# Optimization experiments

Hardware: AMD Instinct MI355X
Metric: run time of the kernel (lower is better)

The kernel has to match this reference:

```python
import jax, jax.numpy as jnp
import numpy as np

V = 32            # number_variables
K = 16            # degree + 1 spline coefficients per pair
DEG = 3           # cubic B-spline order for basis evaluation
LO, HI = -5.0, 5.0
SPAN_FACTOR = 0.1
N_SAMPLES = 131072
P_PAIRS = V * (V - 1) // 2  # 496


def bspline_basis(x):
    """Cubic B-spline basis with K clamped-uniform basis functions on the
    span_factor-expanded range [LO - s, HI + s].  x: [N] -> [N, K]."""
    s = SPAN_FACTOR * (HI - LO)
    lo, hi = LO - s, HI + s
    n_break = K - DEG + 1
    inner = jnp.linspace(lo, hi, n_break)
    t = jnp.concatenate([jnp.full((DEG,), lo), inner, jnp.full((DEG,), hi)])  # [K+DEG+1]
    x = jnp.clip(x, lo, hi - 1e-6 * (hi - lo))
    xb = x[:, None]
    # order-0 indicator functions: [N, K+DEG]
    B = ((xb >= t[None, :-1]) & (xb < t[None, 1:])).astype(x.dtype)
    for r in range(1, DEG + 1):
        tl, tr = t[:-(r + 1)], t[r:-1]
        den1 = tr - tl
        left = jnp.where(den1 > 0, (xb - tl) / jnp.where(den1 > 0, den1, 1.0), 0.0)
        tl2, tr2 = t[1:-r], t[r + 1:]
        den2 = tr2 - tl2
        right = jnp.where(den2 > 0, (tr2 - xb) / jnp.where(den2 > 0, den2, 1.0), 0.0)
        B = left * B[:, :-1] + right * B[:, 1:]
    return B  # [N, K]


def setup_inputs() -> dict:
    key = jax.random.key(0)
    k1, k2 = jax.random.split(key)
    inp = jax.random.normal(k1, (N_SAMPLES, V), dtype=jnp.float32)
    # learned spline coefficients, one column per (var, covar) pair,
    # initialized near the module's 0.1 constant init
    params = 0.1 + 0.05 * jax.random.normal(k2, (K, P_PAIRS), dtype=jnp.float32)
    return {"input": inp, "params": params}


def reference(input, params):
    # output[:, v] = input[:, v] + sum_{c < v} lambda_{v,c}(input[:, c]) * input[:, c]
    # In forward (non-inverse) mode every lambda depends only on `input`, so all
    # V*(V-1)/2 pairs are computed in one batched contraction instead of a loop.
    Basis = jax.vmap(bspline_basis)(input.T)  # [V, N, K], basis per covariate column
    idx_v, idx_c = np.tril_indices(V, -1)      # pair order matches params_index = v*(v-1)/2 + c
    P_mat = jnp.zeros((V, K, V), dtype=input.dtype).at[idx_c, :, idx_v].set(params.T)
    contrib = jnp.einsum('cnk,ckv->cnv', Basis, P_mat)   # lambda_{v,c}(x_{n,c})
    out = input + jnp.einsum('cnv,nc->nv', contrib, input)
    return out
```

## Files before the change

### kernel.cpp

```cpp
#include <hip/hip_runtime.h>
#include <hip/hip_bf16.h>


#define PPAIR 496

typedef _Float16 f16x8 __attribute__((ext_vector_type(8)));
typedef float f32x4 __attribute__((ext_vector_type(4)));
typedef unsigned int u32;
typedef unsigned int u32x4 __attribute__((ext_vector_type(4)));

__global__ __launch_bounds__(256) void prep_w2t(const float* __restrict__ params,
                                                unsigned short* __restrict__ w2t) {
    int idx = blockIdx.x * 256 + threadIdx.x;
    int v = idx >> 9;
    int c = (idx >> 4) & 31, k = idx & 15;
    float w = 0.0f;
    if (c < v) w = params[k * PPAIR + (v * (v - 1)) / 2 + c];
    _Float16 h = (_Float16)w;
    w2t[idx] = __builtin_bit_cast(unsigned short, h);
}

__global__ __launch_bounds__(256, 2) void decor_main(const float* __restrict__ xin,
                                                     const unsigned short* __restrict__ w2t,
                                                     float* __restrict__ out) {
    const int tid = threadIdx.x;
    const int wv = tid >> 6;
    const int l = tid & 63;
    const int s = l & 15;
    const int q = l >> 4;
    const int qp = q & 1;
    const int sigma = ((q & 1) << 1) | (q >> 1);

    f16x8 b1[8][2];
    f16x8 b0[4][2];
#pragma unroll
    for (int u = 0; u < 8; ++u) {
#pragma unroll
        for (int e = 0; e < 2; ++e) {
            int t = 2 * u + (qp ? (1 - e) : e);
            b1[u][e] = *(const f16x8*)(w2t + (16 + s) * 512 + t * 32 + q * 8);
            if (u < 4) b0[u][e] = *(const f16x8*)(w2t + s * 512 + t * 32 + q * 8);
        }
    }

    const float xmax = 5.999988f;
    const float sc = 13.0f / 12.0f;

    for (int tile = 0; tile < 4; ++tile) {
        const int S0 = blockIdx.x * 256 + wv * 64 + tile * 16;
        const float* xrow = xin + (S0 + s) * 32 + sigma;
        float xv[8];
#pragma unroll
        for (int u = 0; u < 8; ++u) xv[u] = xrow[4 * u];

        f32x4 acc0 = {0.f, 0.f, 0.f, 0.f};
        f32x4 acc1 = {0.f, 0.f, 0.f, 0.f};

#pragma unroll
        for (int u = 0; u < 8; ++u) {
            float x = xv[u];
            float xc = fminf(fmaxf(x, -6.0f), xmax);
            float uu = fmaf(xc, sc, 6.5f);
            int mi = (int)uu;
            mi = mi < 12 ? mi : 12;
            float mf = (float)mi;
            float r = uu - mf;
            float N0, N1, N2, N3;
            if (__all(mi >= 3 && mi <= 9)) {
                float omr = 1.0f - r;
                float r2 = r * r, r3 = r2 * r;
                float o2 = omr * omr;
                N0 = o2 * omr * (1.0f / 6.0f);
                N3 = r3 * (1.0f / 6.0f);
                N1 = fmaf(0.5f, r3, (2.0f / 3.0f) - r2);
                N2 = 1.0f - N0 - N1 - N3;
            } else {
                float t13 = 13.0f - mf;
                float af = fminf(mf, 1.0f);
                float bf = fminf(mf, 2.0f);
                float cf = fminf(t13, 2.0f);
                float df = fminf(t13, 3.0f);
                float r1 = 1.0f - r;
                float l2 = r + af, rr2 = cf - r;
                float l3 = r + bf, rr3 = df - r;
                float iv = (af == 0.0f) ? 1.0f : 0.5f;
                float T = r1 * iv;
                float M0 = r1 * T;
                float sv = l2 * T;
                float iv2 = (cf == 1.0f) ? 1.0f : 0.5f;
                float T2 = r * iv2;
                float M1 = fmaf(rr2, T2, sv);
                float M2 = r * T2;
                float iv3 = 0.5f;
                iv3 = (bf == 0.0f) ? 1.0f : iv3;
                iv3 = (bf == 2.0f) ? (1.0f / 3.0f) : iv3;
                T = M0 * iv3;
                N0 = r1 * T;
                sv = l3 * T;
                float g14 = af + cf;
                float iv4 = (g14 == 2.0f) ? 0.5f : (1.0f / 3.0f);
                T = M1 * iv4;
                N1 = fmaf(rr2, T, sv);
                sv = l2 * T;
                float iv5 = 0.5f;
                iv5 = (df == 1.0f) ? 1.0f : iv5;
                iv5 = (df == 3.0f) ? (1.0f / 3.0f) : iv5;
                T = M2 * iv5;
                N2 = fmaf(rr3, T, sv);
                N3 = r * T;
            }
            float g0 = x * N0, g1 = x * N1, g2 = x * N2, g3 = x * N3;
            int e = mi & 1;
            float aa = e ? 0.0f : g0, bb = e ? g0 : g1;
            float cc = e ? g1 : g2, dd = e ? g2 : g3;
            float ee = e ? g3 : 0.0f;
            u32 p0 = __builtin_bit_cast(u32, __builtin_amdgcn_cvt_pkrtz(aa, bb));
            u32 p1 = __builtin_bit_cast(u32, __builtin_amdgcn_cvt_pkrtz(cc, dd));
            u32 p2 = __builtin_bit_cast(u32, __builtin_amdgcn_cvt_pkrtz(ee, 0.0f));
            int w0 = mi >> 1;
            int dlt = w0 & 1;
            u32 C0 = dlt ? 0u : p0;
            u32 C1 = dlt ? p0 : p1;
            u32 C2 = dlt ? p1 : p2;
            u32 C3 = dlt ? p2 : 0u;
            int j0 = (w0 & 6) ^ (qp << 2);
            bool b2 = (j0 & 2) != 0;
            u32 t0 = b2 ? 0u : C0;
            u32 t1 = b2 ? 0u : C1;
            u32 t2 = b2 ? C0 : C2;
            u32 t3 = b2 ? C1 : C3;
            u32 t4 = b2 ? C2 : 0u;
            u32 t5 = b2 ? C3 : 0u;
            bool b4 = (j0 & 4) != 0;
            u32 B0 = b4 ? t4 : t0;
            u32 B1 = b4 ? t5 : t1;
            u32 B2 = b4 ? 0u : t2;
            u32 B3 = b4 ? 0u : t3;
            u32 B4 = b4 ? t0 : t4;
            u32 B5 = b4 ? t1 : t5;
            u32 B6 = b4 ? t2 : 0u;
            u32 B7 = b4 ? t3 : 0u;
            u32 R0 = (u32)__shfl_xor((int)B4, 16);
            u32 R1 = (u32)__shfl_xor((int)B5, 16);
            u32 R2 = (u32)__shfl_xor((int)B6, 16);
            u32 R3 = (u32)__shfl_xor((int)B7, 16);
            u32x4 kp = {B0, B1, B2, B3};
            u32x4 rc = {R0, R1, R2, R3};
            f16x8 ka = __builtin_bit_cast(f16x8, kp);
            f16x8 ra = __builtin_bit_cast(f16x8, rc);
            acc1 = __builtin_amdgcn_mfma_f32_16x16x32_f16(ka, b1[u][0], acc1, 0, 0, 0);
            acc1 = __builtin_amdgcn_mfma_f32_16x16x32_f16(ra, b1[u][1], acc1, 0, 0, 0);
            if (u < 4) {
                acc0 = __builtin_amdgcn_mfma_f32_16x16x32_f16(ka, b0[u][0], acc0, 0, 0, 0);
                acc0 = __builtin_amdgcn_mfma_f32_16x16x32_f16(ra, b0[u][1], acc0, 0, 0, 0);
            }
        }

#pragma unroll
        for (int rI = 0; rI < 4; ++rI) {
            int sample = S0 + q * 4 + rI;
            int base = sample * 32;
            out[base + s]      = xin[base + s]      + acc0[rI];
            out[base + 16 + s] = xin[base + 16 + s] + acc1[rI];
        }
    }
}

extern "C" void kernel_launch(void* const* d_in, const int* in_sizes, int n_in,
                              void* d_out, int out_size, void* d_ws, size_t ws_size,
                              hipStream_t stream) {
    const float* xin = (const float*)d_in[0];
    const float* params = (const float*)d_in[1];
    float* out = (float*)d_out;
    unsigned short* w2t = (unsigned short*)d_ws;

    prep_w2t<<<64, 256, 0, stream>>>(params, w2t);
    decor_main<<<512, 256, 0, stream>>>(xin, w2t, out);
}
```

Baseline: 85.32 us.

## Prefetch next tile inputs, hoist residual loads, raise occupancy to 3 blocks

```diff
diff --git a/kernel.cpp b/kernel.cpp
--- a/kernel.cpp
+++ b/kernel.cpp
@@ -20,7 +20,7 @@
     w2t[idx] = __builtin_bit_cast(unsigned short, h);
 }
 
-__global__ __launch_bounds__(256, 2) void decor_main(const float* __restrict__ xin,
+__global__ __launch_bounds__(256, 3) void decor_main(const float* __restrict__ xin,
                                                      const unsigned short* __restrict__ w2t,
                                                      float* __restrict__ out) {
     const int tid = threadIdx.x;
@@ -43,15 +43,33 @@
         }
     }
 
-    const float xmax = 5.999988f;
     const float sc = 13.0f / 12.0f;
-
+    const int S0w = blockIdx.x * 256 + wv * 64;
+
+    float xv[8];
+    {
+        const float* xr = xin + (S0w + s) * 32 + sigma;
+#pragma unroll
+        for (int u = 0; u < 8; ++u) xv[u] = xr[4 * u];
+    }
+
+#pragma unroll
     for (int tile = 0; tile < 4; ++tile) {
-        const int S0 = blockIdx.x * 256 + wv * 64 + tile * 16;
-        const float* xrow = xin + (S0 + s) * 32 + sigma;
-        float xv[8];
-#pragma unroll
-        for (int u = 0; u < 8; ++u) xv[u] = xrow[4 * u];
+        const int T0 = S0w + tile * 16;
+
+        float xe0[4], xe1[4];
+#pragma unroll
+        for (int rI = 0; rI < 4; ++rI) {
+            int base = (T0 + q * 4 + rI) * 32;
+            xe0[rI] = xin[base + s];
+            xe1[rI] = xin[base + 16 + s];
+        }
+        float xvn[8];
+        if (tile < 3) {
+            const float* xr = xin + (T0 + 16 + s) * 32 + sigma;
+#pragma unroll
+            for (int u = 0; u < 8; ++u) xvn[u] = xr[4 * u];
+        }
 
         f32x4 acc0 = {0.f, 0.f, 0.f, 0.f};
         f32x4 acc1 = {0.f, 0.f, 0.f, 0.f};
@@ -59,10 +77,9 @@
 #pragma unroll
         for (int u = 0; u < 8; ++u) {
             float x = xv[u];
-            float xc = fminf(fmaxf(x, -6.0f), xmax);
-            float uu = fmaf(xc, sc, 6.5f);
+            float uu = fmaf(x, sc, 6.5f);
+            uu = fminf(fmaxf(uu, 0.0f), 12.999987f);
             int mi = (int)uu;
-            mi = mi < 12 ? mi : 12;
             float mf = (float)mi;
             float r = uu - mf;
             float N0, N1, N2, N3;
@@ -158,10 +175,15 @@
 
 #pragma unroll
         for (int rI = 0; rI < 4; ++rI) {
-            int sample = S0 + q * 4 + rI;
+            int sample = T0 + q * 4 + rI;
             int base = sample * 32;
-            out[base + s]      = xin[base + s]      + acc0[rI];
-            out[base + 16 + s] = xin[base + 16 + s] + acc1[rI];
+            out[base + s]      = xe0[rI] + acc0[rI];
+            out[base + 16 + s] = xe1[rI] + acc1[rI];
+        }
+
+        if (tile < 3) {
+#pragma unroll
+            for (int u = 0; u < 8; ++u) xv[u] = xvn[u];
         }
     }
 }
```

Result: no change. 84.62 us (-0.8%).
